# Performance work log

Measured on AMD Instinct MI355X. Metric: run time of the kernel, lower is better.

## Reference

```python
import jax, jax.numpy as jnp
import numpy as np

# ---- static config (matches init_kwargs and NSA hyperparams in source) ----
DIM = 512; HEADS = 8; DH = DIM // HEADS; DEPTH = 2
HH = 28; WW = 28; SEQ = HH * WW            # 784
WIN = 28 * 7                                # sliding window = 196
CBS = 28 * 14; CST = 28 * 7                 # compress block 392, stride 196
SBS = 28 * 14; NSEL = 1                     # selection block 392, top-1
NC = (SEQ - CBS) // CST + 1                 # 3 compressed blocks
NS = SEQ // SBS                             # 2 selection blocks
EPS = 1e-5
BATCH = 8


def _overlap_matrix():
    # fraction of each compressed block overlapping each selection block
    O = np.zeros((NC, NS), np.float32)
    for i in range(NC):
        a, b = i * CST, i * CST + CBS
        for j in range(NS):
            c, d = j * SBS, (j + 1) * SBS
            O[i, j] = max(0, min(b, d) - max(a, c)) / CBS
    return jnp.asarray(O)

OVERLAP = _overlap_matrix()  # [NC, NS]


def setup_inputs() -> dict:
    key = jax.random.key(0)
    ks = jax.random.split(key, 12)
    p = lambda i, shape, s=0.02: (jax.random.normal(ks[i], shape, jnp.float32) * s)
    return {
        "x": jax.random.normal(ks[0], (BATCH, DIM, HH, WW), jnp.float32),
        "pos_emb": jax.random.normal(ks[1], (SEQ,), jnp.float32),
        "attn_norm_g": jnp.ones((DEPTH, DIM), jnp.float32),
        "Wq": p(2, (DEPTH, DIM, HEADS * DH)),
        "Wk": p(3, (DEPTH, DIM, HEADS * DH)),
        "Wv": p(4, (DEPTH, DIM, HEADS * DH)),
        "Wo": p(5, (DEPTH, HEADS * DH, DIM)),
        "Wg": p(6, (DEPTH, DIM, HEADS * 3)),
        "ff_norm_g": jnp.ones((DEPTH, DIM), jnp.float32),
        "ff_norm_b": jnp.zeros((DEPTH, DIM), jnp.float32),
        "ff_w1": p(7, (DEPTH, 4 * DIM, DIM)),
        "ff_b1": jnp.zeros((DEPTH, 4 * DIM), jnp.float32),
        "ff_w2": p(8, (DEPTH, DIM, 4 * DIM)),
        "ff_b2": jnp.zeros((DEPTH, DIM), jnp.float32),
    }


def _sparse_attn(x, g, wq, wk, wv, wo, wg):
    # x: [b, n, d]  -- NSA: sliding window + compressed + top-k block selection
    b, n, d = x.shape
    xr = x * jax.lax.rsqrt(jnp.mean(x * x, -1, keepdims=True) + EPS) * g  # RMSNorm
    q = (xr @ wq).reshape(b, n, HEADS, DH)
    k = (xr @ wk).reshape(b, n, HEADS, DH)
    v = (xr @ wv).reshape(b, n, HEADS, DH)
    scale = DH ** -0.5

    # ---- compressed branch: mean-pool overlapping blocks ----
    ck = jnp.stack([k[:, i * CST:i * CST + CBS].mean(1) for i in range(NC)], 1)  # [b,NC,h,dh]
    cv = jnp.stack([v[:, i * CST:i * CST + CBS].mean(1) for i in range(NC)], 1)
    sc = jnp.einsum('bihd,bjhd->bhij', q, ck) * scale          # [b,h,n,NC]
    pc = jax.nn.softmax(sc, -1)
    out_c = jnp.einsum('bhij,bjhd->bihd', pc, cv)              # [b,n,h,dh]

    # ---- selection branch: importance -> top-k selection blocks -> fine attn ----
    imp = jnp.einsum('bhij,jk->bhik', pc, OVERLAP)             # [b,h,n,NS]
    _, sel = jax.lax.top_k(imp, NSEL)                          # [b,h,n,NSEL]
    selmask = jax.nn.one_hot(sel, NS, dtype=jnp.float32).sum(-2) > 0  # [b,h,n,NS]
    blk = jnp.arange(n) // SBS                                 # token -> selection block
    tokmask = selmask[..., blk]                                # [b,h,n,n]
    sf = jnp.einsum('bihd,bjhd->bhij', q, k) * scale           # full fine scores (shared)
    neg = jnp.finfo(sf.dtype).min
    ps = jax.nn.softmax(jnp.where(tokmask, sf, neg), -1)
    out_s = jnp.einsum('bhij,bjhd->bihd', ps, v)

    # ---- sliding window branch ----
    idx = jnp.arange(n)
    winmask = jnp.abs(idx[:, None] - idx[None, :]) < WIN       # [n,n]
    pw = jax.nn.softmax(jnp.where(winmask, sf, neg), -1)
    out_w = jnp.einsum('bhij,bjhd->bihd', pw, v)

    # ---- per-head learned gates over the 3 branches ----
    gates = jax.nn.sigmoid(xr @ wg).reshape(b, n, HEADS, 3)
    o = (gates[..., 0:1] * out_c + gates[..., 1:2] * out_s + gates[..., 2:3] * out_w)
    return o.reshape(b, n, HEADS * DH) @ wo


def _ff(x, g, bb, w1, b1, w2, b2):
    # x: [b,c,h,w]; LayerNorm over channel dim, then 1x1 conv -> GELU -> 1x1 conv
    mean = x.mean(1, keepdims=True)
    var = jnp.var(x, 1, keepdims=True)
    xn = (x - mean) / jnp.sqrt(var + EPS) * g[None, :, None, None] + bb[None, :, None, None]
    h1 = jax.nn.gelu(jnp.einsum('bchw,oc->bohw', xn, w1) + b1[None, :, None, None], approximate=False)
    return jnp.einsum('bchw,oc->bohw', h1, w2) + b2[None, :, None, None]


def reference(x, pos_emb, attn_norm_g, Wq, Wk, Wv, Wo, Wg,
              ff_norm_g, ff_norm_b, ff_w1, ff_b1, ff_w2, ff_b2):
    b, c, h, w = x.shape
    x = x + pos_emb[:h * w].reshape(1, 1, h, w)
    for l in range(DEPTH):
        s = x.reshape(b, c, h * w).transpose(0, 2, 1)          # b (h w) c
        s = _sparse_attn(s, attn_norm_g[l], Wq[l], Wk[l], Wv[l], Wo[l], Wg[l]) + s
        x = s.transpose(0, 2, 1).reshape(b, c, h, w)
        x = _ff(x, ff_norm_g[l], ff_norm_b[l], ff_w1[l], ff_b1[l], ff_w2[l], ff_b2[l]) + x
    return x
```

## Files before the change

### kernel.cpp

```cpp
#include <hip/hip_runtime.h>
#include <hip/hip_bf16.h>
#include <math.h>

#define B_      8
#define DIMC    512
#define SEQ_    784
#define HEADS_  8
#define DH_     64
#define NTOK    (B_*SEQ_)
#define QLD     1560
#define WIN_    196
#define CBS_    392
#define CST_    196
#define NC_     3
#define EPSF    1e-5f
#define FF_     2048
#define TQ_     28

typedef __hip_bfloat16 bf16_t;
typedef __attribute__((ext_vector_type(8))) short bf16x8;
typedef __attribute__((ext_vector_type(4))) float floatx4;
typedef __attribute__((ext_vector_type(4))) unsigned int uintx4;
typedef __attribute__((ext_vector_type(2))) unsigned int uintx2;

__device__ __forceinline__ float wsum(float x){
#pragma unroll
  for (int o = 32; o; o >>= 1) x += __shfl_xor(x, o, 64);
  return x;
}
__device__ __forceinline__ float geluf(float x){
  return 0.5f * x * (1.0f + erff(x * 0.70710678118654752f));
}
__device__ __forceinline__ float sigmoidf_(float x){
  return 1.0f / (1.0f + __expf(-x));
}
__device__ __forceinline__ void gload16(const bf16_t* g, bf16_t* l){
  __builtin_amdgcn_global_load_lds(
      (const __attribute__((address_space(1))) void*)g,
      (__attribute__((address_space(3))) void*)l, 16, 0, 0);
}

__global__ __launch_bounds__(256) void k_init(const float* __restrict__ xin,
                                              const float* __restrict__ pos,
                                              float* __restrict__ X){
  __shared__ float tl[32][33];
  int blk = blockIdx.x;
  int ct = blk & 15;
  int pt = (blk >> 4) % 25;
  int b  = blk / (16 * 25);
  int p0 = pt * 32, c0 = ct * 32;
  int tx = threadIdx.x & 31, ty = threadIdx.x >> 5;
#pragma unroll
  for (int i = 0; i < 4; i++){
    int p = p0 + tx;
    if (p < SEQ_) tl[ty + i * 8][tx] = xin[((long)(b * DIMC + c0 + ty + i * 8)) * SEQ_ + p];
  }
  __syncthreads();
#pragma unroll
  for (int i = 0; i < 4; i++){
    int p = p0 + ty + i * 8;
    if (p < SEQ_)
      X[((long)(b * SEQ_ + p)) * DIMC + c0 + tx] = tl[tx][ty + i * 8] + pos[p];
  }
}

__global__ __launch_bounds__(256) void k_final(const float* __restrict__ X,
                                               float* __restrict__ out){
  __shared__ float tl[32][33];
  int blk = blockIdx.x;
  int ct = blk & 15;
  int pt = (blk >> 4) % 25;
  int b  = blk / (16 * 25);
  int p0 = pt * 32, c0 = ct * 32;
  int tx = threadIdx.x & 31, ty = threadIdx.x >> 5;
#pragma unroll
  for (int i = 0; i < 4; i++){
    int p = p0 + ty + i * 8;
    if (p < SEQ_) tl[ty + i * 8][tx] = X[((long)(b * SEQ_ + p)) * DIMC + c0 + tx];
  }
  __syncthreads();
#pragma unroll
  for (int i = 0; i < 4; i++){
    int p = p0 + tx;
    if (p < SEQ_)
      out[((long)(b * DIMC + c0 + ty + i * 8)) * SEQ_ + p] = tl[tx][ty + i * 8];
  }
}

__global__ __launch_bounds__(256) void k_wconv1(const float* __restrict__ Wq,
                                                const float* __restrict__ Wk,
                                                const float* __restrict__ Wv,
                                                const float* __restrict__ Wg,
                                                bf16_t* __restrict__ Wb){
  __shared__ float tl[32][33];
  int blk = blockIdx.x;
  int kt = blk & 15;
  int ntf = (blk >> 4) % 49;
  int l = blk / (16 * 49);
  int n0 = ntf * 32, k0 = kt * 32;
  int tx = threadIdx.x & 31, ty = threadIdx.x >> 5;
#pragma unroll
  for (int i = 0; i < 4; i++){
    int n = n0 + tx, k = k0 + ty + i * 8;
    float v = 0.0f;
    if (n < 1536){
      int which = n >> 9, nn = n & 511;
      const float* W = (which == 0) ? Wq : ((which == 1) ? Wk : Wv);
      v = W[((long)(l * 512 + k)) * 512 + nn];
    } else if (n < QLD){
      v = Wg[((long)(l * 512 + k)) * 24 + (n - 1536)];
    }
    tl[ty + i * 8][tx] = v;
  }
  __syncthreads();
#pragma unroll
  for (int i = 0; i < 4; i++){
    int n = n0 + ty + i * 8, k = k0 + tx;
    if (n < QLD)
      Wb[((long)(l * QLD + n)) * 512 + k] = __float2bfloat16(tl[tx][ty + i * 8]);
  }
}

__global__ __launch_bounds__(256) void k_wconv2(const float* __restrict__ Wo,
                                                bf16_t* __restrict__ Wb){
  __shared__ float tl[32][33];
  int blk = blockIdx.x;
  int kt = blk & 15;
  int ntf = (blk >> 4) & 15;
  int l = blk >> 8;
  int n0 = ntf * 32, k0 = kt * 32;
  int tx = threadIdx.x & 31, ty = threadIdx.x >> 5;
#pragma unroll
  for (int i = 0; i < 4; i++)
    tl[ty + i * 8][tx] = Wo[((long)(l * 512 + k0 + ty + i * 8)) * 512 + n0 + tx];
  __syncthreads();
#pragma unroll
  for (int i = 0; i < 4; i++)
    Wb[((long)(l * 512 + n0 + ty + i * 8)) * 512 + k0 + tx] = __float2bfloat16(tl[tx][ty + i * 8]);
}

__global__ __launch_bounds__(256) void k_cast(const float* __restrict__ src,
                                              bf16_t* __restrict__ dst){
  int idx = blockIdx.x * 256 + threadIdx.x;
  dst[idx] = __float2bfloat16(src[idx]);
}

__global__ __launch_bounds__(256) void k_zero(uintx4* __restrict__ p){
  p[blockIdx.x * 256 + threadIdx.x] = (uintx4){0u, 0u, 0u, 0u};
}

__global__ __launch_bounds__(256) void k_rms(const float* __restrict__ X,
                                             const float* __restrict__ g,
                                             bf16_t* __restrict__ XR){
  int tok = blockIdx.x;
  int tid = threadIdx.x;
  const float* xr = X + (long)tok * DIMC;
  float v0 = xr[tid], v1 = xr[tid + 256];
  float ss = v0 * v0 + v1 * v1;
  ss = wsum(ss);
  __shared__ float red[4];
  if ((tid & 63) == 0) red[tid >> 6] = ss;
  __syncthreads();
  float tot = red[0] + red[1] + red[2] + red[3];
  float r = rsqrtf(tot * (1.0f / DIMC) + EPSF);
  XR[(long)tok * DIMC + tid]       = __float2bfloat16(v0 * r * g[tid]);
  XR[(long)tok * DIMC + tid + 256] = __float2bfloat16(v1 * r * g[tid + 256]);
}

__global__ __launch_bounds__(256) void k_ln(const float* __restrict__ X,
                                            const float* __restrict__ g,
                                            const float* __restrict__ bb,
                                            bf16_t* __restrict__ XN){
  int tok = blockIdx.x;
  int tid = threadIdx.x;
  const float* xr = X + (long)tok * DIMC;
  float v0 = xr[tid], v1 = xr[tid + 256];
  float s = v0 + v1;
  float q = v0 * v0 + v1 * v1;
  s = wsum(s); q = wsum(q);
  __shared__ float r1[4], r2[4];
  if ((tid & 63) == 0){ r1[tid >> 6] = s; r2[tid >> 6] = q; }
  __syncthreads();
  float ts = r1[0] + r1[1] + r1[2] + r1[3];
  float tq = r2[0] + r2[1] + r2[2] + r2[3];
  float mean = ts * (1.0f / DIMC);
  float var  = tq * (1.0f / DIMC) - mean * mean;
  float rinv = rsqrtf(var + EPSF);
  XN[(long)tok * DIMC + tid]       = __float2bfloat16((v0 - mean) * rinv * g[tid]       + bb[tid]);
  XN[(long)tok * DIMC + tid + 256] = __float2bfloat16((v1 - mean) * rinv * g[tid + 256] + bb[tid + 256]);
}

template<int OUTBF, int ACT, int BM, int TN, int BK>
__global__ __launch_bounds__(256) void k_mgemm(const bf16_t* __restrict__ A,
                                               const bf16_t* __restrict__ Bm,
                                               float* Cf,
                                               bf16_t* Cb,
                                               const float* __restrict__ bias,
                                               const float* res,
                                               int N, int K, int ldc,
                                               bf16_t* VTo){
  constexpr int MTILES = NTOK / BM;
  constexpr int MPX  = (MTILES + 7) / 8;
  constexpr int MF   = BM / 32;
  constexpr int NF   = TN / 32;
  constexpr int KS   = BK / 32;
  constexpr int RPB2 = 512 / BK;
  constexpr int LPR  = BK / 8;
  constexpr int ABLK = (BM * BK) / 512;
  constexpr int BBLK = (TN * BK) / 512;
  constexpr int TOT  = ABLK + BBLK;
  constexpr int PW   = TOT / 4;
  static_assert(TOT % 4 == 0, "stage blocks must split across 4 waves");

  int id = blockIdx.x;
  int xcd = id & 7;
  int j = id >> 3;
  int nt = j / MPX;
  int mt = xcd * MPX + (j - nt * MPX);
  if (mt >= MTILES) return;
  int bm = mt * BM, bn = nt * TN;

  __shared__ bf16_t As[2][BM][BK];
  __shared__ bf16_t Bs[2][TN][BK];
  int tid = threadIdx.x;
  int w = tid >> 6, lane = tid & 63;
  int wm = (w & 1) * (BM / 2), wn = (w >> 1) * (TN / 2);
  int quad = lane >> 4, l16 = lane & 15;

  int lr = lane / LPR, lc = (lane % LPR) * 8;
  const bf16_t* gsrc[PW];
  bf16_t* ldst0[PW];
  bf16_t* ldst1[PW];
#pragma unroll
  for (int i = 0; i < PW; i++){
    int bi = w * PW + i;
    if (bi < ABLK){
      gsrc[i]  = A + (long)(bm + bi * RPB2 + lr) * K + lc;
      ldst0[i] = &As[0][bi * RPB2][0];
      ldst1[i] = &As[1][bi * RPB2][0];
    } else {
      int bj = bi - ABLK;
      int r = bn + bj * RPB2 + lr; if (r >= N) r = N - 1;
      gsrc[i]  = Bm + (long)r * K + lc;
      ldst0[i] = &Bs[0][bj * RPB2][0];
      ldst1[i] = &Bs[1][bj * RPB2][0];
    }
  }

  floatx4 acc[MF][NF];
#pragma unroll
  for (int i = 0; i < MF; i++)
#pragma unroll
    for (int jj = 0; jj < NF; jj++) acc[i][jj] = (floatx4)(0.0f);

#define MG_STAGE0(ko) do { _Pragma("unroll") \
    for (int i_ = 0; i_ < PW; i_++) gload16(gsrc[i_] + (ko), ldst0[i_]); } while (0)
#define MG_STAGE1(ko) do { _Pragma("unroll") \
    for (int i_ = 0; i_ < PW; i_++) gload16(gsrc[i_] + (ko), ldst1[i_]); } while (0)
#define MG_COMPUTE(BUFI) do { _Pragma("unroll") \
    for (int ks_ = 0; ks_ < KS; ks_++){ \
      bf16x8 af_[MF], bf_[NF]; \
      _Pragma("unroll") \
      for (int m_ = 0; m_ < MF; m_++) \
        af_[m_] = *(bf16x8*)&As[BUFI][wm + m_ * 16 + l16][ks_ * 32 + quad * 8]; \
      _Pragma("unroll") \
      for (int f_ = 0; f_ < NF; f_++) \
        bf_[f_] = *(bf16x8*)&Bs[BUFI][wn + f_ * 16 + l16][ks_ * 32 + quad * 8]; \
      _Pragma("unroll") \
      for (int m_ = 0; m_ < MF; m_++) \
        _Pragma("unroll") \
        for (int f_ = 0; f_ < NF; f_++) \
          acc[m_][f_] = __builtin_amdgcn_mfma_f32_16x16x32_bf16(af_[m_], bf_[f_], acc[m_][f_], 0, 0, 0); \
    } } while (0)

  int nch = K / BK;
  MG_STAGE0(0);
  __syncthreads();
  for (int ch = 0; ch < nch; ch += 2){
    MG_STAGE1((ch + 1) * BK);
    MG_COMPUTE(0);
    __syncthreads();
    if (ch + 2 < nch) MG_STAGE0((ch + 2) * BK);
    MG_COMPUTE(1);
    __syncthreads();
  }
#undef MG_STAGE0
#undef MG_STAGE1
#undef MG_COMPUTE

#pragma unroll
  for (int tm = 0; tm < MF; tm++){
#pragma unroll
    for (int tn = 0; tn < NF; tn++){
      int ncol = bn + wn + tn * 16 + l16;
      if (ncol >= N) continue;
#pragma unroll
      for (int reg = 0; reg < 4; reg++){
        long mrow = bm + wm + tm * 16 + quad * 4 + reg;
        float v = acc[tm][tn][reg];
        if (bias) v += bias[ncol];
        if (ACT == 1) v = geluf(v);
        long off = mrow * (long)ldc + ncol;
        if (res) v += res[off];
        if (OUTBF){
          Cb[off] = __float2bfloat16(v);
          if (VTo && ncol >= 1024 && ncol < 1536){
            int bb2 = (int)(mrow / SEQ_);
            int tok = (int)(mrow - (long)bb2 * SEQ_);
            VTo[((long)(bb2 * 512 + (ncol - 1024))) * 800 + tok] = __float2bfloat16(v);
          }
        }
        else       Cf[off] = v;
      }
    }
  }
}

__global__ __launch_bounds__(256) void k_cpool(const bf16_t* __restrict__ qkvg,
                                               float* __restrict__ ck,
                                               float* __restrict__ cv){
  int blk = blockIdx.x;
  int cs = blk & 7;
  int bj = blk >> 3;
  int j = bj % NC_;
  int b = bj / NC_;
  int tid = threadIdx.x;
  int seg = tid & 15;
  int rg  = tid >> 4;
  __shared__ float part[16][128];
  const bf16_t* base = qkvg + ((long)b * SEQ_ + (long)j * CST_) * QLD + 512 + cs * 128;
  float acc[8] = {0.f,0.f,0.f,0.f,0.f,0.f,0.f,0.f};
  for (int r = rg; r < CBS_; r += 16){
    uintx4 v = *(const uintx4*)(base + (long)r * QLD + seg * 8);
    bf16_t tmp[8]; *(uintx4*)tmp = v;
#pragma unroll
    for (int q = 0; q < 8; q++) acc[q] += __bfloat162float(tmp[q]);
  }
#pragma unroll
  for (int q = 0; q < 8; q++) part[rg][seg * 8 + q] = acc[q];
  __syncthreads();
  if (tid < 128){
    float s = 0.f;
#pragma unroll
    for (int g = 0; g < 16; g++) s += part[g][tid];
    s *= (1.0f / CBS_);
    int gch = cs * 128 + tid;
    if (gch < 512) ck[bj * DIMC + gch] = s;
    else           cv[bj * DIMC + (gch - 512)] = s;
  }
}

__global__ __launch_bounds__(256) void k_attn(const bf16_t* __restrict__ qkvg,
                                              const float* __restrict__ ck,
                                              const float* __restrict__ cv,
                                              const bf16_t* __restrict__ vtg,
                                              bf16_t* __restrict__ oattn){
  int tid = threadIdx.x;
  int w = tid >> 6, lane = tid & 63;
  int quad = lane >> 4, l16 = lane & 15;
  int id = blockIdx.x;
  int xcd = id & 7;
  int j = id >> 3;
  int bh = xcd * 8 + (j / 28);
  int i0 = (j % 28) * TQ_;
  int h = bh & 7, b = bh >> 3;
  const float scale = 0.125f;

  __shared__ bf16_t Qs[32][72];
  __shared__ bf16_t Ks[2][64][72];
  __shared__ bf16_t Wcw[2][32][72];
  __shared__ bf16_t Wcs[2][32][72];
  __shared__ float outc_s[28][64];
  __shared__ int   sel_s[28];
  __shared__ float cw_s[28], cs_s[28], g1_s[28], g2_s[28];
  __shared__ float red_s[4][4][16];

  const long rowBase = (long)b * SEQ_ * QLD + h * 64;

  if (tid < 224){
    int q = tid >> 3, seg = tid & 7;
    uintx4 qv = *(const uintx4*)(qkvg + rowBase + (long)(i0 + q) * QLD + seg * 8);
    *(uintx4*)&Qs[q][seg * 8] = qv;
  } else {
    int u = tid - 224;
    int r = 28 + (u >> 3), seg = u & 7;
    *(uintx4*)&Qs[r][seg * 8] = (uintx4){0u, 0u, 0u, 0u};
  }
  for (int t = tid; t < 2 * 4 * 72; t += 256){
    int bufi = t / (4 * 72);
    int r = 28 + (t / 72) % 4;
    int c = t % 72;
    Wcw[bufi][r][c] = __float2bfloat16(0.0f);
    Wcs[bufi][r][c] = __float2bfloat16(0.0f);
  }
  __syncthreads();

  int r0i = tid >> 3, s0i = tid & 7;
  int r1i = 32 + r0i;
  uintx4 kreg0 = *(const uintx4*)(qkvg + rowBase + (long)r0i * QLD + 512 + s0i * 8);
  uintx4 kreg1 = *(const uintx4*)(qkvg + rowBase + (long)r1i * QLD + 512 + s0i * 8);

  {
    const float* CKp = ck + (long)b * NC_ * DIMC + h * 64 + lane;
    const float* CVp = cv + (long)b * NC_ * DIMC + h * 64 + lane;
    float k0 = CKp[0], k1 = CKp[512], k2 = CKp[1024];
    float v0 = CVp[0], v1 = CVp[512], v2 = CVp[1024];
#pragma unroll
    for (int qp = 0; qp < 7; qp++){
      int qg = w * 7 + qp;
      float qd = __bfloat162float(Qs[qg][lane]);
      float s0 = wsum(qd * k0) * scale;
      float s1 = wsum(qd * k1) * scale;
      float s2 = wsum(qd * k2) * scale;
      float m3 = fmaxf(s0, fmaxf(s1, s2));
      float e0 = __expf(s0 - m3), e1 = __expf(s1 - m3), e2 = __expf(s2 - m3);
      float inv = 1.0f / (e0 + e1 + e2);
      const bf16_t* grow = qkvg + (long)(b * SEQ_ + i0 + qg) * QLD + 1536 + h * 3;
      float g0 = sigmoidf_(__bfloat162float(grow[0]));
      float g1v = sigmoidf_(__bfloat162float(grow[1]));
      float g2v = sigmoidf_(__bfloat162float(grow[2]));
      outc_s[qg][lane] = g0 * (e0 * v0 + e1 * v1 + e2 * v2) * inv;
      int selv = (s2 > s0) ? 1 : 0;
      if (lane == 0){ sel_s[qg] = selv; g1_s[qg] = g1v; g2_s[qg] = g2v; }
    }
  }

  bf16x8 a00 = *(bf16x8*)&Qs[l16][quad * 8];
  bf16x8 a01 = *(bf16x8*)&Qs[l16][32 + quad * 8];
  bf16x8 a10 = *(bf16x8*)&Qs[16 + l16][quad * 8];
  bf16x8 a11 = *(bf16x8*)&Qs[16 + l16][32 + quad * 8];

  __syncthreads();

  int nsel1 = 0;
#pragma unroll
  for (int q = 0; q < 28; q++) nsel1 += sel_s[q];
  const bool any0 = (nsel1 < 28), any1 = (nsel1 > 0);

  int sel0i = sel_s[l16];
  int sel1i = (l16 < 12) ? sel_s[16 + l16] : 0;
  bool sv0 = (sel0i != 0), sv1 = (sel1i != 0);
  int iq0 = i0 + l16, iq1 = i0 + 16 + l16;
  float sw0 = 0.f, ss0 = 0.f, sw1 = 0.f, ss1 = 0.f;

  const bf16_t* vbase = vtg + ((long)(b * 512 + h * 64 + w * 16 + l16)) * 800;
  floatx4 ow0 = (floatx4)(0.0f), ow1 = (floatx4)(0.0f);
  floatx4 os0 = (floatx4)(0.0f), os1 = (floatx4)(0.0f);

  for (int ch = 0; ch < 13; ch++){
    int buf = ch & 1;
    int K0 = ch * 64;
    bool wact = (K0 + 63 >= i0 - 195) && (K0 <= i0 + 222);
    bool sact = ((K0 <= 391) && any0) || ((K0 + 63 >= 392) && any1);
    bool pact = wact || sact;
    *(uintx4*)&Ks[buf][r0i][s0i * 8] = kreg0;
    *(uintx4*)&Ks[buf][r1i][s0i * 8] = kreg1;
    __syncthreads();
    if (ch + 1 < 13){
      int c0n = (ch + 1) * 64;
      int t0 = c0n + r0i; if (t0 > 783) t0 = 783;
      int t1 = c0n + r1i; if (t1 > 783) t1 = 783;
      kreg0 = *(const uintx4*)(qkvg + rowBase + (long)t0 * QLD + 512 + s0i * 8);
      kreg1 = *(const uintx4*)(qkvg + rowBase + (long)t1 * QLD + 512 + s0i * 8);
    }
    int tv0 = K0 + quad * 8;      if (tv0 > 792) tv0 = 792;
    int tv1 = K0 + 32 + quad * 8; if (tv1 > 792) tv1 = 792;
    bf16x8 bv0 = *(const bf16x8*)(vbase + tv0);
    bf16x8 bv1 = *(const bf16x8*)(vbase + tv1);
    if (pact){
      bf16x8 k0 = *(bf16x8*)&Ks[buf][w * 16 + l16][quad * 8];
      bf16x8 k1 = *(bf16x8*)&Ks[buf][w * 16 + l16][32 + quad * 8];
      floatx4 d0 = (floatx4)(0.0f), d1 = (floatx4)(0.0f);
      d0 = __builtin_amdgcn_mfma_f32_16x16x32_bf16(k0, a00, d0, 0, 0, 0);
      d0 = __builtin_amdgcn_mfma_f32_16x16x32_bf16(k1, a01, d0, 0, 0, 0);
      d1 = __builtin_amdgcn_mfma_f32_16x16x32_bf16(k0, a10, d1, 0, 0, 0);
      d1 = __builtin_amdgcn_mfma_f32_16x16x32_bf16(k1, a11, d1, 0, 0, 0);
      int kb = K0 + w * 16 + quad * 4;
      float ex0[4], ex1[4];
#pragma unroll
      for (int r = 0; r < 4; r++){
        ex0[r] = __expf(d0[r] * scale);
        ex1[r] = __expf(d1[r] * scale);
      }
      int kloc = w * 16 + quad * 4;
      if (wact){
        union { bf16_t hh[4]; uintx2 v; } pw0, pw1;
#pragma unroll
        for (int r = 0; r < 4; r++){
          int key = kb + r;
          bool valid = key < 784;
          float vw0 = (valid && key >= iq0 - 195 && key <= iq0 + 195) ? ex0[r] : 0.0f;
          float vw1 = (valid && key >= iq1 - 195 && key <= iq1 + 195) ? ex1[r] : 0.0f;
          sw0 += vw0; sw1 += vw1;
          pw0.hh[r] = __float2bfloat16(vw0);
          pw1.hh[r] = __float2bfloat16(vw1);
        }
        if (kb < 784){
          *(uintx2*)&Wcw[buf][l16][kloc] = pw0.v;
          if (l16 < 12) *(uintx2*)&Wcw[buf][16 + l16][kloc] = pw1.v;
        }
      }
      if (sact){
        union { bf16_t hh[4]; uintx2 v; } ps0, ps1;
#pragma unroll
        for (int r = 0; r < 4; r++){
          int key = kb + r;
          bool valid = key < 784;
          float vs0 = (valid && ((key >= 392) == sv0)) ? ex0[r] : 0.0f;
          float vs1 = (valid && ((key >= 392) == sv1)) ? ex1[r] : 0.0f;
          ss0 += vs0; ss1 += vs1;
          ps0.hh[r] = __float2bfloat16(vs0);
          ps1.hh[r] = __float2bfloat16(vs1);
        }
        if (kb < 784){
          *(uintx2*)&Wcs[buf][l16][kloc] = ps0.v;
          if (l16 < 12) *(uintx2*)&Wcs[buf][16 + l16][kloc] = ps1.v;
        }
      }
    }
    __syncthreads();
    if (wact){
#pragma unroll
      for (int ks = 0; ks < 2; ks++){
        bf16x8 bv = ks ? bv1 : bv0;
        bf16x8 aw0 = *(bf16x8*)&Wcw[buf][l16][ks * 32 + quad * 8];
        bf16x8 aw1 = *(bf16x8*)&Wcw[buf][16 + l16][ks * 32 + quad * 8];
        ow0 = __builtin_amdgcn_mfma_f32_16x16x32_bf16(aw0, bv, ow0, 0, 0, 0);
        ow1 = __builtin_amdgcn_mfma_f32_16x16x32_bf16(aw1, bv, ow1, 0, 0, 0);
      }
    }
    if (sact){
#pragma unroll
      for (int ks = 0; ks < 2; ks++){
        bf16x8 bv = ks ? bv1 : bv0;
        bf16x8 as0 = *(bf16x8*)&Wcs[buf][l16][ks * 32 + quad * 8];
        bf16x8 as1 = *(bf16x8*)&Wcs[buf][16 + l16][ks * 32 + quad * 8];
        os0 = __builtin_amdgcn_mfma_f32_16x16x32_bf16(as0, bv, os0, 0, 0, 0);
        os1 = __builtin_amdgcn_mfma_f32_16x16x32_bf16(as1, bv, os1, 0, 0, 0);
      }
    }
  }

  sw0 += __shfl_xor(sw0, 16, 64); sw0 += __shfl_xor(sw0, 32, 64);
  ss0 += __shfl_xor(ss0, 16, 64); ss0 += __shfl_xor(ss0, 32, 64);
  sw1 += __shfl_xor(sw1, 16, 64); sw1 += __shfl_xor(sw1, 32, 64);
  ss1 += __shfl_xor(ss1, 16, 64); ss1 += __shfl_xor(ss1, 32, 64);
  if (quad == 0){
    red_s[w][0][l16] = sw0; red_s[w][1][l16] = ss0;
    red_s[w][2][l16] = sw1; red_s[w][3][l16] = ss1;
  }
  __syncthreads();
  if (tid < 28){
    int q = tid, t = q >> 4, l = q & 15;
    float sw = 0.f, ss = 0.f;
#pragma unroll
    for (int wv = 0; wv < 4; wv++){ sw += red_s[wv][2 * t][l]; ss += red_s[wv][2 * t + 1][l]; }
    cw_s[q] = g2_s[q] / sw;
    cs_s[q] = g1_s[q] / ss;
  }
  __syncthreads();

  int d = w * 16 + l16;
#pragma unroll
  for (int reg = 0; reg < 4; reg++){
    int q = quad * 4 + reg;
    float o = cw_s[q] * ow0[reg] + cs_s[q] * os0[reg] + outc_s[q][d];
    oattn[((long)(b * SEQ_ + i0 + q)) * DIMC + h * 64 + d] = __float2bfloat16(o);
    int q2 = q + 16;
    if (q2 < 28){
      float o2 = cw_s[q2] * ow1[reg] + cs_s[q2] * os1[reg] + outc_s[q2][d];
      oattn[((long)(b * SEQ_ + i0 + q2)) * DIMC + h * 64 + d] = __float2bfloat16(o2);
    }
  }
}

extern "C" void kernel_launch(void* const* d_in, const int* in_sizes, int n_in,
                              void* d_out, int out_size, void* d_ws, size_t ws_size,
                              hipStream_t stream){
  const float* xin  = (const float*)d_in[0];
  const float* pos  = (const float*)d_in[1];
  const float* angm = (const float*)d_in[2];
  const float* Wq   = (const float*)d_in[3];
  const float* Wk   = (const float*)d_in[4];
  const float* Wv   = (const float*)d_in[5];
  const float* Wo   = (const float*)d_in[6];
  const float* Wg   = (const float*)d_in[7];
  const float* fng  = (const float*)d_in[8];
  const float* fnb  = (const float*)d_in[9];
  const float* fw1  = (const float*)d_in[10];
  const float* fb1  = (const float*)d_in[11];
  const float* fw2  = (const float*)d_in[12];
  const float* fb2  = (const float*)d_in[13];

  char* cw = (char*)d_ws;
  float* X = (float*)cw;             cw += (long)NTOK * 512 * 4;
  bf16_t* XRb = (bf16_t*)cw;         cw += (long)NTOK * 512 * 2;
  bf16_t* OAb = (bf16_t*)cw;         cw += (long)NTOK * 512 * 2;
  bf16_t* SH  = (bf16_t*)cw;         cw += (long)NTOK * FF_ * 2;
  float* CK = (float*)cw;            cw += (long)B_ * NC_ * DIMC * 4;
  float* CV = (float*)cw;            cw += (long)B_ * NC_ * DIMC * 4;
  bf16_t* Wqkvgb = (bf16_t*)cw;      cw += (long)2 * QLD * 512 * 2;
  bf16_t* WOb    = (bf16_t*)cw;      cw += (long)2 * 512 * 512 * 2;
  bf16_t* FW1b   = (bf16_t*)cw;      cw += (long)2 * FF_ * 512 * 2;
  bf16_t* FW2b   = (bf16_t*)cw;      cw += (long)2 * 512 * FF_ * 2;
  bf16_t* VTb    = (bf16_t*)cw;      cw += (long)B_ * 512 * 800 * 2;
  bf16_t* BUFb = SH;
  bf16_t* H1b  = SH;

  k_wconv1<<<2 * 49 * 16, 256, 0, stream>>>(Wq, Wk, Wv, Wg, Wqkvgb);
  k_wconv2<<<2 * 16 * 16, 256, 0, stream>>>(Wo, WOb);
  k_cast<<<(2 * FF_ * 512) / 256, 256, 0, stream>>>(fw1, FW1b);
  k_cast<<<(2 * 512 * FF_) / 256, 256, 0, stream>>>(fw2, FW2b);

  k_zero<<<1600, 256, 0, stream>>>((uintx4*)VTb);

  k_init<<<8 * 25 * 16, 256, 0, stream>>>(xin, pos, X);

  for (int l = 0; l < 2; l++){
    k_rms<<<NTOK, 256, 0, stream>>>(X, angm + (long)l * DIMC, XRb);

    k_mgemm<1, 0, 128, 128, 32><<<13 * 56, 256, 0, stream>>>(
        XRb, Wqkvgb + (long)l * QLD * 512, nullptr, BUFb, nullptr, nullptr,
        QLD, 512, QLD, VTb);

    k_cpool<<<B_ * NC_ * 8, 256, 0, stream>>>(BUFb, CK, CV);

    k_attn<<<8 * 8 * 28, 256, 0, stream>>>(BUFb, CK, CV, VTb, OAb);

    k_mgemm<0, 0, 64, 64, 64><<<8 * 104, 256, 0, stream>>>(
        OAb, WOb + (long)l * 512 * 512, X, nullptr, nullptr, X,
        512, 512, 512, nullptr);

    k_ln<<<NTOK, 256, 0, stream>>>(X, fng + (long)l * DIMC, fnb + (long)l * DIMC, XRb);

    k_mgemm<1, 1, 128, 128, 32><<<16 * 56, 256, 0, stream>>>(
        XRb, FW1b + (long)l * FF_ * 512, nullptr, H1b, fb1 + (long)l * FF_, nullptr,
        FF_, 512, FF_, nullptr);
    k_mgemm<0, 0, 64, 64, 64><<<8 * 104, 256, 0, stream>>>(
        H1b, FW2b + (long)l * 512 * FF_, X, nullptr, fb2 + (long)l * DIMC, X,
        512, FF_, 512, nullptr);
  }

  k_final<<<8 * 25 * 16, 256, 0, stream>>>(X, (float*)d_out);
}
```

Measured before the change: 580.1 us.

## Keep two LDS stages in flight with explicit vmcnt waits in GEMM

Reworks the GEMM main loop so both double-buffer stages are issued up front and the next stage's global-to-LDS loads stay in flight during compute. Fine-grained s_waitcnt vmcnt(4)/vmcnt(0) plus raw s_barrier replace __syncthreads, which waits for all outstanding loads. The goal is to overlap memory latency with MFMA work. It relies on exactly 4 loads per thread per stage, enforced by a static_assert, and adds more barriers per iteration.

```diff
diff --git a/kernel.cpp b/kernel.cpp
--- a/kernel.cpp
+++ b/kernel.cpp
@@ -211,6 +211,7 @@
   constexpr int TOT  = ABLK + BBLK;
   constexpr int PW   = TOT / 4;
   static_assert(TOT % 4 == 0, "stage blocks must split across 4 waves");
+  static_assert(PW == 4, "vmcnt(4) counting assumes 4 gload16 per thread per stage");
 
   int id = blockIdx.x;
   int xcd = id & 7;
@@ -272,21 +273,45 @@
         for (int f_ = 0; f_ < NF; f_++) \
           acc[m_][f_] = __builtin_amdgcn_mfma_f32_16x16x32_bf16(af_[m_], bf_[f_], acc[m_][f_], 0, 0, 0); \
     } } while (0)
+#define MG_WAIT4()  do { asm volatile("s_waitcnt vmcnt(4)" ::: "memory"); \
+                         __builtin_amdgcn_sched_barrier(0); } while (0)
+#define MG_WAIT0()  do { asm volatile("s_waitcnt vmcnt(0)" ::: "memory"); \
+                         __builtin_amdgcn_sched_barrier(0); } while (0)
+#define MG_BAR()    do { asm volatile("" ::: "memory"); \
+                         __builtin_amdgcn_s_barrier(); \
+                         asm volatile("" ::: "memory"); } while (0)
 
   int nch = K / BK;
   MG_STAGE0(0);
-  __syncthreads();
+  MG_STAGE1(BK);
+  MG_WAIT4();
+  MG_BAR();
   for (int ch = 0; ch < nch; ch += 2){
-    MG_STAGE1((ch + 1) * BK);
     MG_COMPUTE(0);
-    __syncthreads();
-    if (ch + 2 < nch) MG_STAGE0((ch + 2) * BK);
+    MG_BAR();
+    if (ch + 2 < nch){
+      MG_STAGE0((ch + 2) * BK);
+      MG_WAIT4();
+    } else {
+      MG_WAIT0();
+    }
+    MG_BAR();
     MG_COMPUTE(1);
-    __syncthreads();
+    MG_BAR();
+    if (ch + 3 < nch){
+      MG_STAGE1((ch + 3) * BK);
+      MG_WAIT4();
+    } else if (ch + 2 < nch){
+      MG_WAIT0();
+    }
+    MG_BAR();
   }
 #undef MG_STAGE0
 #undef MG_STAGE1
 #undef MG_COMPUTE
+#undef MG_WAIT4
+#undef MG_WAIT0
+#undef MG_BAR
 
 #pragma unroll
   for (int tm = 0; tm < MF; tm++){
```

After: 547.0 us. -5.7%, faster.
